# Kernel optimization log

Hardware: AMD Instinct MI355X
Metric: run time of the kernel (lower is better)

The kernel has to match this reference:

```python
import jax, jax.numpy as jnp
import numpy as np

B, S, H = 128, 512, 768      # batch, seq, encoder hidden
NL = 42                      # len(LABEL_TO_ID)
LD = 300                     # label_dim
DK, DV = 64, 768             # K_dim, V_dim
HID = 768                    # opt['hidden_dim']
P = 512                      # max_seq_length == pos_indicator
INF = 1e12                   # constant.INFINITY_NUMBER
NEG = -1e9


def gelu(x):
    return 0.5 * x * (1.0 + jax.lax.erf(x * 0.7071067811865476))


def setup_inputs() -> dict:
    key = jax.random.key(0)
    ks = jax.random.split(key, 24)
    sc = 0.02
    return {
        "inputs": jax.random.normal(ks[0], (B, S, H), jnp.float32),
        "pos_ids": jax.random.randint(ks[1], (B, S), 0, 53),
        "dep_ids": jax.random.randint(ks[2], (B, S), 0, 42),
        "subj_pos": jax.random.randint(ks[3], (B, S), 0, P + 1),
        "obj_pos": jax.random.randint(ks[4], (B, S), 0, P + 1),
        "adj": jnp.zeros((1, 1, 1), jnp.float32),  # unused by forward
        # stacked per-label Q/K projections (41 = NL-1 labels, label 0 excluded)
        "WQ": jax.random.normal(ks[5], (NL - 1, DK, H), jnp.float32) * sc,
        "bQ": jax.random.normal(ks[6], (NL - 1, DK), jnp.float32) * sc,
        "WK": jax.random.normal(ks[7], (NL - 1, DK, LD), jnp.float32) * sc,
        "bK": jax.random.normal(ks[8], (NL - 1, DK), jnp.float32) * sc,
        "WV_w": jax.random.normal(ks[9], (DV, H), jnp.float32) * sc,
        "WV_b": jax.random.normal(ks[10], (DV,), jnp.float32) * sc,
        "Wout_w": jax.random.normal(ks[11], (H, DV), jnp.float32) * sc,
        "Wout_b": jax.random.normal(ks[12], (H,), jnp.float32) * sc,
        "ln_g": jnp.ones((H,), jnp.float32),
        "ln_b": jnp.zeros((H,), jnp.float32),
        "label_emb": jax.random.normal(ks[13], (NL, LD), jnp.float32) * sc,
        "feat_w": jax.random.normal(ks[14], (HID, 3 * H), jnp.float32) * sc,
        "feat_b": jax.random.normal(ks[15], (HID,), jnp.float32) * sc,
        "out_w": jax.random.normal(ks[16], (LD, HID), jnp.float32) * sc,
        "out_b": jax.random.normal(ks[17], (LD,), jnp.float32) * sc,
    }


def reference(inputs, pos_ids, dep_ids, subj_pos, obj_pos, adj,
              WQ, bQ, WK, bK, WV_w, WV_b, Wout_w, Wout_b, ln_g, ln_b,
              label_emb, feat_w, feat_b, out_w, out_b):
    dt = inputs.dtype
    # combined attention mask (bool OR, as torch bool+bool): entity markers + padding
    mask = (subj_pos == P) | (obj_pos == P) | (pos_ids == 0)   # [B,S]

    # --- LabelAttention: 41-loop collapses to one fused projection ---
    lab = label_emb[1:NL]                                      # [41,LD] labels 1..41
    kvec = jnp.einsum('ld,lkd->lk', lab, WK) + bK              # [41,DK] per-label keys
    # scores_sum[b,s] = sum_l (x W_Q_l^T + b_Q_l) . k_l  /sqrt(dk)  + 41*mask*NEG
    w_eff = jnp.einsum('lk,lkh->h', kvec, WQ)                  # [H]
    c = jnp.sum(kvec * bQ)                                     # scalar
    scores = (inputs @ w_eff + c) / 8.0                        # sqrt(DK)=8; [B,S]
    scores = scores + (NL - 1) * mask.astype(dt) * NEG
    attn = jax.nn.softmax(scores, axis=-1)                     # [B,S]

    wv = inputs @ WV_w.T + WV_b                                # [B,S,DV]
    ctx = jnp.einsum('bs,bsd->bd', attn, wv)                   # [B,DV]
    ctx = gelu(ctx @ Wout_w.T + Wout_b)                        # [B,H]
    mu = ctx.mean(-1, keepdims=True)
    var = ((ctx - mu) ** 2).mean(-1, keepdims=True)
    ctx = (ctx - mu) / jnp.sqrt(var + 1e-5) * ln_g + ln_b

    # --- entity max pooling (mask True where NOT part of entity) ---
    sm = (subj_pos != P)[:, :, None]
    om = (obj_pos != P)[:, :, None]
    subj_out = jnp.where(sm, -INF, inputs).max(axis=1)         # [B,H]
    obj_out = jnp.where(om, -INF, inputs).max(axis=1)          # [B,H]

    feats = jnp.concatenate([subj_out, obj_out, ctx], axis=-1)  # [B,3H]
    feats = gelu(feats @ feat_w.T + feat_b)                     # [B,HID]
    feats = gelu(feats @ out_w.T + out_b)                       # [B,LD]

    logits = feats @ label_emb.T                                # [B,42]
    return logits, ctx
```

## Files before the change

### kernel.cpp

```cpp
#include <hip/hip_runtime.h>
#include <math.h>

#define BB 128
#define SS 512
#define HH 768
#define PPOS 512
#define NEGC (-1.0e9f)
#define NINF (-1.0e12f)

#define OFF_KVEC   0
#define OFF_WEFF   2624
#define OFF_C      3392
#define OFF_SCORES 4096
#define OFF_CAT    0
#define OFF_POOLED 294912
#define OFF_PP     393216
#define OFF_PS     1179648
#define OFF_PO     1966080
#define OFF_CTXA   393216
#define OFF_CTXB   491520
#define OFF_F1     589824
#define OFF_F2     688128

__device__ __forceinline__ float gelu_f(float x) {
    return 0.5f * x * (1.0f + erff(x * 0.70710678118654752f));
}
__device__ __forceinline__ float dot4(float4 a, float4 b) {
    return a.x*b.x + a.y*b.y + a.z*b.z + a.w*b.w;
}

template<int K4, int ACT, int MT>
__global__ __launch_bounds__(256) void k_mm(const float* __restrict__ A,
        const float* __restrict__ W, const float* __restrict__ bias,
        float* __restrict__ C, int M, int N) {
    int lane = threadIdx.x & 63;
    int wave = (blockIdx.x * 256 + threadIdx.x) >> 6;
    int ntn = (N + 15) >> 4;
    int m0 = (wave / ntn) * MT;
    if (m0 >= M) return;
    int n0 = ((wave % ntn) << 4) + (lane >> 2);
    int ks = lane & 3;
    bool nvalid = (n0 < N);
    const float4* A4 = (const float4*)A;
    const float4* w_row = (const float4*)W + (size_t)(nvalid ? n0 : 0) * K4;
    const float4* ar = A4 + (size_t)m0 * K4;
    float acc[MT];
    #pragma unroll
    for (int r = 0; r < MT; ++r) acc[r] = 0.f;
    #pragma unroll 4
    for (int j = ks; j < K4; j += 4) {
        float4 wv = w_row[j];
        #pragma unroll
        for (int r = 0; r < MT; ++r) acc[r] += dot4(ar[(size_t)r * K4 + j], wv);
    }
    #pragma unroll
    for (int r = 0; r < MT; ++r) {
        acc[r] += __shfl_xor(acc[r], 1, 64);
        acc[r] += __shfl_xor(acc[r], 2, 64);
    }
    if (ks == 0 && nvalid) {
        float b = bias ? bias[n0] : 0.f;
        #pragma unroll
        for (int r = 0; r < MT; ++r) {
            float v = acc[r] + b;
            if (ACT == 1) v = gelu_f(v);
            C[(size_t)(m0 + r) * N + n0] = v;
        }
    }
}

__global__ __launch_bounds__(256) void k_kvec2(const float* __restrict__ label_emb,
        const float* __restrict__ WK, const float* __restrict__ bK,
        float* __restrict__ ws) {
    if (blockIdx.x < 3) ws[OFF_WEFF + blockIdx.x * 256 + threadIdx.x] = 0.f;
    if (blockIdx.x == 3 && threadIdx.x == 0) ws[OFF_C] = 0.f;
    int lane = threadIdx.x & 63;
    int idx = (blockIdx.x * 256 + threadIdx.x) >> 6;
    int l = idx >> 6;
    const float4* lab4 = (const float4*)(label_emb + (size_t)(l + 1) * 300);
    const float4* wk4  = (const float4*)(WK + (size_t)idx * 300);
    float acc = dot4(lab4[lane], wk4[lane]);
    if (lane < 11) acc += dot4(lab4[64 + lane], wk4[64 + lane]);
    #pragma unroll
    for (int off = 32; off > 0; off >>= 1) acc += __shfl_xor(acc, off, 64);
    if (lane == 0) ws[OFF_KVEC + idx] = acc + bK[idx];
}

__global__ __launch_bounds__(256) void k_weff2(const float* __restrict__ WQ,
        const float* __restrict__ bQ, float* __restrict__ ws) {
    int lane = threadIdx.x & 63;
    int w = (blockIdx.x * 256 + threadIdx.x) >> 6;
    if (w < 492) {
        int jc = w / 12, hg = w % 12;
        int h = hg * 64 + lane;
        const float* wq = WQ + (size_t)(jc * 64) * HH + h;
        const float* kv = ws + OFF_KVEC + jc * 64;
        float acc = 0.f;
        #pragma unroll 8
        for (int j = 0; j < 64; ++j) acc += kv[j] * wq[(size_t)j * HH];
        atomicAdd(&ws[OFF_WEFF + h], acc);
    } else if (w == 492) {
        float acc = 0.f;
        for (int j = lane; j < 2624; j += 64) acc += ws[OFF_KVEC + j] * bQ[j];
        #pragma unroll
        for (int off = 32; off > 0; off >>= 1) acc += __shfl_xor(acc, off, 64);
        if (lane == 0) atomicAdd(&ws[OFF_C], acc);
    }
}

__global__ __launch_bounds__(256) void k_scores(const float* __restrict__ inputs,
        const int* __restrict__ pos_ids, const int* __restrict__ subj_pos,
        const int* __restrict__ obj_pos, float* __restrict__ ws) {
    int wave = threadIdx.x >> 6, lane = threadIdx.x & 63;
    const float4* in4 = (const float4*)inputs;
    const float4* w4  = (const float4*)(ws + OFF_WEFF);
    float c = ws[OFF_C];
    float4 w0 = w4[lane], w1 = w4[64 + lane], w2 = w4[128 + lane];
    int wid = blockIdx.x * 4 + wave;
    for (int i = 0; i < 8; ++i) {
        int row = wid + 8192 * i;
        const float4* r4 = in4 + (size_t)row * 192;
        float acc = dot4(r4[lane], w0) + dot4(r4[64 + lane], w1) + dot4(r4[128 + lane], w2);
        #pragma unroll
        for (int off = 32; off > 0; off >>= 1) acc += __shfl_down(acc, off, 64);
        if (lane == 0) {
            bool m = (subj_pos[row] == PPOS) | (obj_pos[row] == PPOS) | (pos_ids[row] == 0);
            float sc = (acc + c) * 0.125f;
            if (m) sc += 41.0f * NEGC;
            ws[OFF_SCORES + row] = sc;
        }
    }
}

__global__ __launch_bounds__(192) void k_pool(const float* __restrict__ inputs,
        const int* __restrict__ subj_pos, const int* __restrict__ obj_pos,
        float* __restrict__ ws) {
    __shared__ float red[256];
    __shared__ float al[64];
    __shared__ int lsf[64];
    __shared__ int lof[64];
    int chunk = blockIdx.x, b = blockIdx.y, t = threadIdx.x;
    int s0 = chunk * 64;
    const float* sc = ws + OFF_SCORES + (size_t)b * SS;
    float v0 = sc[t], v1 = sc[t + 192], v2 = (t < 128) ? sc[t + 384] : NINF;
    red[t] = fmaxf(fmaxf(v0, v1), v2);
    if (t >= 128) { }
    if (t < 64) red[t + 192] = NINF;
    __syncthreads();
    for (int s2 = 128; s2 > 0; s2 >>= 1) {
        if (t < s2) red[t] = fmaxf(red[t], red[t + s2]);
        __syncthreads();
    }
    float m = red[0];
    __syncthreads();
    float e0 = expf(v0 - m) + expf(v1 - m) + ((t < 128) ? expf(v2 - m) : 0.f);
    red[t] = e0;
    if (t < 64) red[t + 192] = 0.f;
    __syncthreads();
    for (int s2 = 128; s2 > 0; s2 >>= 1) {
        if (t < s2) red[t] += red[t + s2];
        __syncthreads();
    }
    float inv = 1.0f / red[0];
    if (t < 64) {
        int gs = b * SS + s0 + t;
        al[t]  = expf(sc[s0 + t] - m) * inv;
        lsf[t] = (subj_pos[gs] == PPOS);
        lof[t] = (obj_pos[gs] == PPOS);
    }
    __syncthreads();
    const float4* in4 = (const float4*)inputs;
    float4 pool = make_float4(0.f, 0.f, 0.f, 0.f);
    float4 smax = make_float4(NINF, NINF, NINF, NINF);
    float4 omax = make_float4(NINF, NINF, NINF, NINF);
    for (int s = 0; s < 64; ++s) {
        float4 x = in4[((size_t)(b * SS + s0 + s)) * 192 + t];
        float a = al[s];
        pool.x += a * x.x; pool.y += a * x.y; pool.z += a * x.z; pool.w += a * x.w;
        if (lsf[s]) {
            smax.x = fmaxf(smax.x, x.x); smax.y = fmaxf(smax.y, x.y);
            smax.z = fmaxf(smax.z, x.z); smax.w = fmaxf(smax.w, x.w);
        }
        if (lof[s]) {
            omax.x = fmaxf(omax.x, x.x); omax.y = fmaxf(omax.y, x.y);
            omax.z = fmaxf(omax.z, x.z); omax.w = fmaxf(omax.w, x.w);
        }
    }
    size_t o = (size_t)(b * 8 + chunk) * 192 + t;
    ((float4*)(ws + OFF_PP))[o] = pool;
    ((float4*)(ws + OFF_PS))[o] = smax;
    ((float4*)(ws + OFF_PO))[o] = omax;
}

__global__ void k_reduce(float* __restrict__ ws) {
    int i = blockIdx.x * 256 + threadIdx.x;
    int b = i / HH, h = i - b * HH;
    float p = 0.f, sm = NINF, om = NINF;
    #pragma unroll
    for (int j = 0; j < 8; ++j) {
        int o = (b * 8 + j) * HH + h;
        p += ws[OFF_PP + o];
        sm = fmaxf(sm, ws[OFF_PS + o]);
        om = fmaxf(om, ws[OFF_PO + o]);
    }
    ws[OFF_POOLED + i] = p;
    ws[OFF_CAT + (size_t)b * 2304 + h] = sm;
    ws[OFF_CAT + (size_t)b * 2304 + 768 + h] = om;
}

__global__ void k_ln(const float* __restrict__ ln_g, const float* __restrict__ ln_b,
                     float* __restrict__ ws, float* __restrict__ out) {
    __shared__ float red[256];
    __shared__ float red2[256];
    int b = blockIdx.x, t = threadIdx.x;
    const float* x = ws + OFF_CTXB + (size_t)b * HH;
    float a0 = x[t], a1 = x[t + 256], a2 = x[t + 512];
    red[t]  = a0 + a1 + a2;
    red2[t] = a0 * a0 + a1 * a1 + a2 * a2;
    __syncthreads();
    for (int s2 = 128; s2 > 0; s2 >>= 1) {
        if (t < s2) { red[t] += red[t + s2]; red2[t] += red2[t + s2]; }
        __syncthreads();
    }
    float mu  = red[0] * (1.0f / 768.0f);
    float var = red2[0] * (1.0f / 768.0f) - mu * mu;
    float inv = rsqrtf(var + 1e-5f);
    float* o = out + 5376 + (size_t)b * HH;
    float* cc = ws + OFF_CAT + (size_t)b * 2304 + 1536;
    float r0 = (a0 - mu) * inv * ln_g[t]       + ln_b[t];
    float r1 = (a1 - mu) * inv * ln_g[t + 256] + ln_b[t + 256];
    float r2 = (a2 - mu) * inv * ln_g[t + 512] + ln_b[t + 512];
    o[t] = r0; o[t + 256] = r1; o[t + 512] = r2;
    cc[t] = r0; cc[t + 256] = r1; cc[t + 512] = r2;
}

extern "C" void kernel_launch(void* const* d_in, const int* in_sizes, int n_in,
                              void* d_out, int out_size, void* d_ws, size_t ws_size,
                              hipStream_t stream) {
    const float* inputs    = (const float*)d_in[0];
    const int*   pos_ids   = (const int*)d_in[1];
    const int*   subj_pos  = (const int*)d_in[3];
    const int*   obj_pos   = (const int*)d_in[4];
    const float* WQ        = (const float*)d_in[6];
    const float* bQ        = (const float*)d_in[7];
    const float* WK        = (const float*)d_in[8];
    const float* bK        = (const float*)d_in[9];
    const float* WV_w      = (const float*)d_in[10];
    const float* WV_b      = (const float*)d_in[11];
    const float* Wout_w    = (const float*)d_in[12];
    const float* Wout_b    = (const float*)d_in[13];
    const float* ln_g      = (const float*)d_in[14];
    const float* ln_b      = (const float*)d_in[15];
    const float* label_emb = (const float*)d_in[16];
    const float* feat_w    = (const float*)d_in[17];
    const float* feat_b    = (const float*)d_in[18];
    const float* out_w     = (const float*)d_in[19];
    const float* out_b     = (const float*)d_in[20];
    float* out = (float*)d_out;
    float* ws  = (float*)d_ws;

    k_kvec2  <<<656, 256, 0, stream>>>(label_emb, WK, bK, ws);
    k_weff2  <<<124, 256, 0, stream>>>(WQ, bQ, ws);
    k_scores <<<2048, 256, 0, stream>>>(inputs, pos_ids, subj_pos, obj_pos, ws);
    k_pool   <<<dim3(8, BB), 192, 0, stream>>>(inputs, subj_pos, obj_pos, ws);
    k_reduce <<<384, 256, 0, stream>>>(ws);
    k_mm<192,0,2><<<768, 256, 0, stream>>>(ws + OFF_POOLED, WV_w, WV_b, ws + OFF_CTXA, BB, HH);
    k_mm<192,1,2><<<768, 256, 0, stream>>>(ws + OFF_CTXA, Wout_w, Wout_b, ws + OFF_CTXB, BB, HH);
    k_ln     <<<BB, 256, 0, stream>>>(ln_g, ln_b, ws, out);
    k_mm<576,1,2><<<768, 256, 0, stream>>>(ws + OFF_CAT, feat_w, feat_b, ws + OFF_F1, BB, HH);
    k_mm<192,1,2><<<304, 256, 0, stream>>>(ws + OFF_F1, out_w, out_b, ws + OFF_F2, BB, 300);
    k_mm<75,0,2><<<48, 256, 0, stream>>>(ws + OFF_F2, label_emb, nullptr, out, BB, 42);
}
```

Baseline: 474.8 us.

## Fuse score computation with softmax-weighted and entity max pooling in one pass

Merges the score kernel and the pooling kernel into one kernel that reads each input row once. For each row it computes the attention score, its unnormalised exponential, the weighted sum and the subject/object max pools. Normalisation is deferred by storing per-chunk exponential sums, which the reduce kernel adds up and divides by. This removes a second full pass over the large input tensor. The cost is dropping the max-subtraction in the softmax and using the fast __expf, which risks overflow or lost precision if scores get large.

```diff
diff --git a/kernel.cpp b/kernel.cpp
--- a/kernel.cpp
+++ b/kernel.cpp
@@ -11,12 +11,12 @@
 #define OFF_KVEC   0
 #define OFF_WEFF   2624
 #define OFF_C      3392
-#define OFF_SCORES 4096
 #define OFF_CAT    0
 #define OFF_POOLED 294912
 #define OFF_PP     393216
 #define OFF_PS     1179648
 #define OFF_PO     1966080
+#define OFF_PZ     2752512
 #define OFF_CTXA   393216
 #define OFF_CTXB   491520
 #define OFF_F1     589824
@@ -108,102 +108,114 @@
     }
 }
 
-__global__ __launch_bounds__(256) void k_scores(const float* __restrict__ inputs,
+__global__ __launch_bounds__(256) void k_fused(const float* __restrict__ inputs,
         const int* __restrict__ pos_ids, const int* __restrict__ subj_pos,
         const int* __restrict__ obj_pos, float* __restrict__ ws) {
-    int wave = threadIdx.x >> 6, lane = threadIdx.x & 63;
-    const float4* in4 = (const float4*)inputs;
-    const float4* w4  = (const float4*)(ws + OFF_WEFF);
+    __shared__ float l_pe[4][768];
+    __shared__ float l_sm[4][768];
+    __shared__ float l_om[4][768];
+    __shared__ float l_z[4];
+    __shared__ int l_mask[64];
+    int chunk = blockIdx.x, b = blockIdx.y;
+    int t = threadIdx.x, wave = t >> 6, lane = t & 63;
+    int row0 = b * SS + chunk * 64;
+    if (t < 64) {
+        int g = row0 + t;
+        int sp = subj_pos[g], op = obj_pos[g], pi = pos_ids[g];
+        int m = ((sp == PPOS) | (op == PPOS) | (pi == 0)) ? 1 : 0;
+        if (sp == PPOS) m |= 2;
+        if (op == PPOS) m |= 4;
+        l_mask[t] = m;
+    }
+    const float4* w4 = (const float4*)(ws + OFF_WEFF);
     float c = ws[OFF_C];
     float4 w0 = w4[lane], w1 = w4[64 + lane], w2 = w4[128 + lane];
-    int wid = blockIdx.x * 4 + wave;
-    for (int i = 0; i < 8; ++i) {
-        int row = wid + 8192 * i;
-        const float4* r4 = in4 + (size_t)row * 192;
-        float acc = dot4(r4[lane], w0) + dot4(r4[64 + lane], w1) + dot4(r4[128 + lane], w2);
-        #pragma unroll
-        for (int off = 32; off > 0; off >>= 1) acc += __shfl_down(acc, off, 64);
-        if (lane == 0) {
-            bool m = (subj_pos[row] == PPOS) | (obj_pos[row] == PPOS) | (pos_ids[row] == 0);
-            float sc = (acc + c) * 0.125f;
-            if (m) sc += 41.0f * NEGC;
-            ws[OFF_SCORES + row] = sc;
-        }
-    }
-}
-
-__global__ __launch_bounds__(192) void k_pool(const float* __restrict__ inputs,
-        const int* __restrict__ subj_pos, const int* __restrict__ obj_pos,
-        float* __restrict__ ws) {
-    __shared__ float red[256];
-    __shared__ float al[64];
-    __shared__ int lsf[64];
-    __shared__ int lof[64];
-    int chunk = blockIdx.x, b = blockIdx.y, t = threadIdx.x;
-    int s0 = chunk * 64;
-    const float* sc = ws + OFF_SCORES + (size_t)b * SS;
-    float v0 = sc[t], v1 = sc[t + 192], v2 = (t < 128) ? sc[t + 384] : NINF;
-    red[t] = fmaxf(fmaxf(v0, v1), v2);
-    if (t >= 128) { }
-    if (t < 64) red[t + 192] = NINF;
-    __syncthreads();
-    for (int s2 = 128; s2 > 0; s2 >>= 1) {
-        if (t < s2) red[t] = fmaxf(red[t], red[t + s2]);
-        __syncthreads();
-    }
-    float m = red[0];
-    __syncthreads();
-    float e0 = expf(v0 - m) + expf(v1 - m) + ((t < 128) ? expf(v2 - m) : 0.f);
-    red[t] = e0;
-    if (t < 64) red[t + 192] = 0.f;
-    __syncthreads();
-    for (int s2 = 128; s2 > 0; s2 >>= 1) {
-        if (t < s2) red[t] += red[t + s2];
-        __syncthreads();
-    }
-    float inv = 1.0f / red[0];
-    if (t < 64) {
-        int gs = b * SS + s0 + t;
-        al[t]  = expf(sc[s0 + t] - m) * inv;
-        lsf[t] = (subj_pos[gs] == PPOS);
-        lof[t] = (obj_pos[gs] == PPOS);
-    }
     __syncthreads();
     const float4* in4 = (const float4*)inputs;
-    float4 pool = make_float4(0.f, 0.f, 0.f, 0.f);
-    float4 smax = make_float4(NINF, NINF, NINF, NINF);
-    float4 omax = make_float4(NINF, NINF, NINF, NINF);
-    for (int s = 0; s < 64; ++s) {
-        float4 x = in4[((size_t)(b * SS + s0 + s)) * 192 + t];
-        float a = al[s];
-        pool.x += a * x.x; pool.y += a * x.y; pool.z += a * x.z; pool.w += a * x.w;
-        if (lsf[s]) {
-            smax.x = fmaxf(smax.x, x.x); smax.y = fmaxf(smax.y, x.y);
-            smax.z = fmaxf(smax.z, x.z); smax.w = fmaxf(smax.w, x.w);
-        }
-        if (lof[s]) {
-            omax.x = fmaxf(omax.x, x.x); omax.y = fmaxf(omax.y, x.y);
-            omax.z = fmaxf(omax.z, x.z); omax.w = fmaxf(omax.w, x.w);
-        }
-    }
-    size_t o = (size_t)(b * 8 + chunk) * 192 + t;
-    ((float4*)(ws + OFF_PP))[o] = pool;
-    ((float4*)(ws + OFF_PS))[o] = smax;
-    ((float4*)(ws + OFF_PO))[o] = omax;
+    float4 pe0 = make_float4(0.f, 0.f, 0.f, 0.f);
+    float4 pe1 = pe0, pe2 = pe0;
+    float4 sm0 = make_float4(NINF, NINF, NINF, NINF);
+    float4 sm1 = sm0, sm2 = sm0, om0 = sm0, om1 = sm0, om2 = sm0;
+    float z = 0.f;
+    int rbase = wave * 16;
+    #pragma unroll 4
+    for (int r = 0; r < 16; ++r) {
+        int s = rbase + r;
+        const float4* x4 = in4 + (size_t)(row0 + s) * 192;
+        float4 x0 = x4[lane], x1 = x4[64 + lane], x2 = x4[128 + lane];
+        float acc = dot4(x0, w0) + dot4(x1, w1) + dot4(x2, w2);
+        #pragma unroll
+        for (int off = 32; off > 0; off >>= 1) acc += __shfl_xor(acc, off, 64);
+        int mk = l_mask[s];
+        float e = (mk & 1) ? 0.f : __expf((acc + c) * 0.125f);
+        z += e;
+        pe0.x += e * x0.x; pe0.y += e * x0.y; pe0.z += e * x0.z; pe0.w += e * x0.w;
+        pe1.x += e * x1.x; pe1.y += e * x1.y; pe1.z += e * x1.z; pe1.w += e * x1.w;
+        pe2.x += e * x2.x; pe2.y += e * x2.y; pe2.z += e * x2.z; pe2.w += e * x2.w;
+        if (mk & 2) {
+            sm0.x = fmaxf(sm0.x, x0.x); sm0.y = fmaxf(sm0.y, x0.y);
+            sm0.z = fmaxf(sm0.z, x0.z); sm0.w = fmaxf(sm0.w, x0.w);
+            sm1.x = fmaxf(sm1.x, x1.x); sm1.y = fmaxf(sm1.y, x1.y);
+            sm1.z = fmaxf(sm1.z, x1.z); sm1.w = fmaxf(sm1.w, x1.w);
+            sm2.x = fmaxf(sm2.x, x2.x); sm2.y = fmaxf(sm2.y, x2.y);
+            sm2.z = fmaxf(sm2.z, x2.z); sm2.w = fmaxf(sm2.w, x2.w);
+        }
+        if (mk & 4) {
+            om0.x = fmaxf(om0.x, x0.x); om0.y = fmaxf(om0.y, x0.y);
+            om0.z = fmaxf(om0.z, x0.z); om0.w = fmaxf(om0.w, x0.w);
+            om1.x = fmaxf(om1.x, x1.x); om1.y = fmaxf(om1.y, x1.y);
+            om1.z = fmaxf(om1.z, x1.z); om1.w = fmaxf(om1.w, x1.w);
+            om2.x = fmaxf(om2.x, x2.x); om2.y = fmaxf(om2.y, x2.y);
+            om2.z = fmaxf(om2.z, x2.z); om2.w = fmaxf(om2.w, x2.w);
+        }
+    }
+    ((float4*)l_pe[wave])[lane] = pe0;
+    ((float4*)l_pe[wave])[64 + lane] = pe1;
+    ((float4*)l_pe[wave])[128 + lane] = pe2;
+    ((float4*)l_sm[wave])[lane] = sm0;
+    ((float4*)l_sm[wave])[64 + lane] = sm1;
+    ((float4*)l_sm[wave])[128 + lane] = sm2;
+    ((float4*)l_om[wave])[lane] = om0;
+    ((float4*)l_om[wave])[64 + lane] = om1;
+    ((float4*)l_om[wave])[128 + lane] = om2;
+    if (lane == 0) l_z[wave] = z;
+    __syncthreads();
+    if (t < 192) {
+        float4 p = make_float4(0.f, 0.f, 0.f, 0.f);
+        float4 s = make_float4(NINF, NINF, NINF, NINF);
+        float4 o = s;
+        #pragma unroll
+        for (int w = 0; w < 4; ++w) {
+            float4 vp = ((float4*)l_pe[w])[t];
+            float4 vs = ((float4*)l_sm[w])[t];
+            float4 vo = ((float4*)l_om[w])[t];
+            p.x += vp.x; p.y += vp.y; p.z += vp.z; p.w += vp.w;
+            s.x = fmaxf(s.x, vs.x); s.y = fmaxf(s.y, vs.y);
+            s.z = fmaxf(s.z, vs.z); s.w = fmaxf(s.w, vs.w);
+            o.x = fmaxf(o.x, vo.x); o.y = fmaxf(o.y, vo.y);
+            o.z = fmaxf(o.z, vo.z); o.w = fmaxf(o.w, vo.w);
+        }
+        size_t oo = (size_t)(b * 8 + chunk) * 192 + t;
+        ((float4*)(ws + OFF_PP))[oo] = p;
+        ((float4*)(ws + OFF_PS))[oo] = s;
+        ((float4*)(ws + OFF_PO))[oo] = o;
+    }
+    if (t == 0) ws[OFF_PZ + b * 8 + chunk] = l_z[0] + l_z[1] + l_z[2] + l_z[3];
 }
 
 __global__ void k_reduce(float* __restrict__ ws) {
     int i = blockIdx.x * 256 + threadIdx.x;
     int b = i / HH, h = i - b * HH;
-    float p = 0.f, sm = NINF, om = NINF;
+    float p = 0.f, sm = NINF, om = NINF, zt = 0.f;
     #pragma unroll
     for (int j = 0; j < 8; ++j) {
         int o = (b * 8 + j) * HH + h;
         p += ws[OFF_PP + o];
         sm = fmaxf(sm, ws[OFF_PS + o]);
         om = fmaxf(om, ws[OFF_PO + o]);
-    }
-    ws[OFF_POOLED + i] = p;
+        zt += ws[OFF_PZ + b * 8 + j];
+    }
+    ws[OFF_POOLED + i] = p / zt;
     ws[OFF_CAT + (size_t)b * 2304 + h] = sm;
     ws[OFF_CAT + (size_t)b * 2304 + 768 + h] = om;
 }
@@ -261,8 +273,7 @@
 
     k_kvec2  <<<656, 256, 0, stream>>>(label_emb, WK, bK, ws);
     k_weff2  <<<124, 256, 0, stream>>>(WQ, bQ, ws);
-    k_scores <<<2048, 256, 0, stream>>>(inputs, pos_ids, subj_pos, obj_pos, ws);
-    k_pool   <<<dim3(8, BB), 192, 0, stream>>>(inputs, subj_pos, obj_pos, ws);
+    k_fused  <<<dim3(8, BB), 256, 0, stream>>>(inputs, pos_ids, subj_pos, obj_pos, ws);
     k_reduce <<<384, 256, 0, stream>>>(ws);
     k_mm<192,0,2><<<768, 256, 0, stream>>>(ws + OFF_POOLED, WV_w, WV_b, ws + OFF_CTXA, BB, HH);
     k_mm<192,1,2><<<768, 256, 0, stream>>>(ws + OFF_CTXA, Wout_w, Wout_b, ws + OFF_CTXB, BB, HH);
```

Measured after the change: 454.4 us. 4.3% less time.
